# Kernel optimization log

Hardware: AMD Instinct MI355X
Metric: run time of the kernel (lower is better)

## Reference

```python
import jax, jax.numpy as jnp
import numpy as np

B, T, NT = 256, 1024, 96  # batch, max seq len, num_tags (incl. start/end)


def setup_inputs() -> dict:
    key = jax.random.key(0)
    k1, k2, k3 = jax.random.split(key, 3)
    h = jax.random.normal(k1, (B, T, NT), dtype=jnp.float32)
    # lengths in [1, T]; force at least one full-length sequence so max_len == T
    lengths = jax.random.randint(k2, (B,), 1, T + 1).at[0].set(T)
    trans = jax.random.normal(k3, (NT, NT), dtype=jnp.float32)  # trans[to, from]
    return {"h": h, "lengths": lengths, "trans": trans}


def reference(h, lengths, trans):
    # CRF forward algorithm (log partition function), masked for variable lengths.
    Bb, Tt, nt = h.shape
    start_tag, end_tag = nt - 2, nt - 1  # start_tag=-2, end_tag=-1
    mask = jnp.arange(Tt)[None, :] < lengths[:, None]  # [B, T]

    score0 = jnp.full((Bb, nt), -10000.0, dtype=h.dtype).at[:, start_tag].set(0.0)

    def step(score, xs):
        h_t, m_t = xs  # h_t: [B, NT], m_t: [B]
        # score[b, j] (prev tag j) + trans[i, j] + emit h_t[b, i] -> [B, NT(i), NT(j)]
        s = score[:, None, :] + trans[None, :, :] + h_t[:, :, None]
        s = jax.nn.logsumexp(s, axis=2)  # [B, NT]
        score = jnp.where(m_t[:, None], s, score)
        return score, None

    score, _ = jax.lax.scan(step, score0, (jnp.swapaxes(h, 0, 1), mask.T))
    # transition into end tag, then final logsumexp over tags -> [B]
    return jax.nn.logsumexp(score + trans[end_tag][None, :], axis=1)
```

## Files before the change

### kernel.cpp

```cpp
#include <hip/hip_runtime.h>

#define Bb 256
#define Tt 1024
#define NT 96
#define PF 8

__global__ __launch_bounds__(256, 1) void crf_fwd_kernel(
    const float* __restrict__ h,
    const int*   __restrict__ lengths,
    const float* __restrict__ trans,
    float* __restrict__ out)
{
    const int b    = blockIdx.x;
    const int tid  = threadIdx.x;
    const int i    = tid >> 1;
    const int q    = tid & 1;
    const int L    = lengths[b];
    const bool active = (i < NT);
    const int wave = tid >> 6;

    __shared__ float p_lds[2][128];
    __shared__ float fin[4];

    float E[48];
    if (active) {
        const float* tr = trans + i * NT + q * 48;
        #pragma unroll
        for (int k = 0; k < 48; ++k) E[k] = __expf(tr[k]);
    } else {
        #pragma unroll
        for (int k = 0; k < 48; ++k) E[k] = 0.0f;
    }

    if (tid < 128) p_lds[0][tid] = (tid == NT - 2) ? 1.0f : 0.0f;

    const float* hb = h + (size_t)b * Tt * NT;

    float hp[PF];
    #pragma unroll
    for (int k = 0; k < PF; ++k)
        hp[k] = active ? hb[(size_t)k * NT + i] : 0.0f;

    const float c  = 4.0f;
    const float Kc = __expf(-c);
    float M = 0.0f;
    float p_keep = 0.0f;

    __syncthreads();

    int cur = 0;
    for (int tb = 0; tb < Tt; tb += PF) {
        #pragma unroll
        for (int k = 0; k < PF; ++k) {
            const int t = tb + k;

            const float p0 = p_lds[cur][0];

            const float4* pv = reinterpret_cast<const float4*>(p_lds[cur] + q * 48);
            float a0 = 0.f, a1 = 0.f, a2 = 0.f, a3 = 0.f;
            #pragma unroll
            for (int m = 0; m < 12; ++m) {
                const float4 p4 = pv[m];
                a0 = fmaf(E[4*m+0], p4.x, a0);
                a1 = fmaf(E[4*m+1], p4.y, a1);
                a2 = fmaf(E[4*m+2], p4.z, a2);
                a3 = fmaf(E[4*m+3], p4.w, a3);
            }
            float v = (a0 + a1) + (a2 + a3);
            v += __shfl_xor(v, 1, 64);

            const float eh = __expf(hp[k]);
            int tn = t + PF; if (tn > Tt - 1) tn = Tt - 1;
            hp[k] = active ? hb[(size_t)tn * NT + i] : 0.0f;

            const float u  = (t == 0) ? 1.0f : Kc * __builtin_amdgcn_rcpf(p0);
            const float w  = v * eh;
            const bool msk = (t < L);
            const float pn = msk ? (w * u) : p_keep;
            M -= msk ? __logf(u) : 0.0f;
            p_keep = pn;

            const int nxt = cur ^ 1;
            if (active && q == 0) p_lds[nxt][i] = pn;

            __syncthreads();
            cur = nxt;
        }
    }

    float term = (active && q == 0) ? p_keep * __expf(trans[(NT - 1) * NT + i]) : 0.0f;
    #pragma unroll
    for (int s = 1; s < 64; s <<= 1) term += __shfl_xor(term, s, 64);
    if ((tid & 63) == 0) fin[wave] = term;
    __syncthreads();
    if (tid == 0) out[b] = M + __logf(fin[0] + fin[1] + fin[2] + fin[3]);
}

extern "C" void kernel_launch(void* const* d_in, const int* in_sizes, int n_in,
                              void* d_out, int out_size, void* d_ws, size_t ws_size,
                              hipStream_t stream) {
    const float* h       = (const float*)d_in[0];
    const int*   lengths = (const int*)d_in[1];
    const float* trans   = (const float*)d_in[2];
    float*       out     = (float*)d_out;
    (void)in_sizes; (void)n_in; (void)out_size; (void)d_ws; (void)ws_size;

    crf_fwd_kernel<<<Bb, 256, 0, stream>>>(h, lengths, trans, out);
}
```

Measured before the change: 405.5 us.

## Batch 16 sequences per wave with bf16 MFMA recurrence and exp prepass

Replaces the per-batch 256-thread FMA recurrence with a single-wave kernel that advances 16 sequences together. Each step is a bf16 MFMA matrix product of the exponentiated transition matrix against the probability vectors held in LDS. Renormalisation happens only every 16 steps, and the emissions are exponentiated in a separate prepass into workspace when one is available. This removes the block-wide barrier per step and the scalar dot products, but the grid drops to 16 one-wave blocks, the bf16 truncation adds precision loss, and the prepass adds a full extra pass over h.

Measured after the change: 783.6 us. 1.93x slower.

```diff
diff --git a/kernel.cpp b/kernel.cpp
--- a/kernel.cpp
+++ b/kernel.cpp
@@ -3,97 +3,173 @@
 #define Bb 256
 #define Tt 1024
 #define NT 96
-#define PF 8
+#define CH 16
+#define CSTR 120
 
-__global__ __launch_bounds__(256, 1) void crf_fwd_kernel(
-    const float* __restrict__ h,
-    const int*   __restrict__ lengths,
-    const float* __restrict__ trans,
-    float* __restrict__ out)
-{
-    const int b    = blockIdx.x;
-    const int tid  = threadIdx.x;
-    const int i    = tid >> 1;
-    const int q    = tid & 1;
-    const int L    = lengths[b];
-    const bool active = (i < NT);
-    const int wave = tid >> 6;
+typedef __attribute__((ext_vector_type(8))) short bf16x8;
+typedef __attribute__((ext_vector_type(4))) float f32x4;
 
-    __shared__ float p_lds[2][128];
-    __shared__ float fin[4];
+__device__ __forceinline__ unsigned short bf16_rne(float f) {
+    unsigned int b = __float_as_uint(f);
+    b += 0x7FFFu + ((b >> 16) & 1u);
+    return (unsigned short)(b >> 16);
+}
 
-    float E[48];
-    if (active) {
-        const float* tr = trans + i * NT + q * 48;
+__global__ void exp_prepass(const float4* __restrict__ src, float4* __restrict__ dst, int n4) {
+    int idx = blockIdx.x * blockDim.x + threadIdx.x;
+    int stride = gridDim.x * blockDim.x;
+    for (int i = idx; i < n4; i += stride) {
+        float4 v = src[i];
+        dst[i] = make_float4(__expf(v.x), __expf(v.y), __expf(v.z), __expf(v.w));
+    }
+}
+
+template <bool PRE>
+__global__ __attribute__((amdgpu_flat_work_group_size(64, 64),
+                          amdgpu_waves_per_eu(1, 1)))
+void crf_mfma_kernel(const float* __restrict__ hsrc,
+                     const int* __restrict__ lengths,
+                     const float* __restrict__ trans,
+                     float* __restrict__ out) {
+    const int b0   = blockIdx.x * CH;
+    const int lane = threadIdx.x;
+    const int c    = lane & 15;
+    const int g    = lane >> 4;
+    const int L    = lengths[b0 + c];
+
+    __shared__ __align__(16) short pbuf[CH * CSTR];
+
+    bf16x8 afrag[6][3];
+    #pragma unroll
+    for (int mt = 0; mt < 6; ++mt) {
+        const float* row = trans + (16 * mt + c) * NT;
         #pragma unroll
-        for (int k = 0; k < 48; ++k) E[k] = __expf(tr[k]);
-    } else {
-        #pragma unroll
-        for (int k = 0; k < 48; ++k) E[k] = 0.0f;
-    }
-
-    if (tid < 128) p_lds[0][tid] = (tid == NT - 2) ? 1.0f : 0.0f;
-
-    const float* hb = h + (size_t)b * Tt * NT;
-
-    float hp[PF];
-    #pragma unroll
-    for (int k = 0; k < PF; ++k)
-        hp[k] = active ? hb[(size_t)k * NT + i] : 0.0f;
-
-    const float c  = 4.0f;
-    const float Kc = __expf(-c);
-    float M = 0.0f;
-    float p_keep = 0.0f;
-
-    __syncthreads();
-
-    int cur = 0;
-    for (int tb = 0; tb < Tt; tb += PF) {
-        #pragma unroll
-        for (int k = 0; k < PF; ++k) {
-            const int t = tb + k;
-
-            const float p0 = p_lds[cur][0];
-
-            const float4* pv = reinterpret_cast<const float4*>(p_lds[cur] + q * 48);
-            float a0 = 0.f, a1 = 0.f, a2 = 0.f, a3 = 0.f;
-            #pragma unroll
-            for (int m = 0; m < 12; ++m) {
-                const float4 p4 = pv[m];
-                a0 = fmaf(E[4*m+0], p4.x, a0);
-                a1 = fmaf(E[4*m+1], p4.y, a1);
-                a2 = fmaf(E[4*m+2], p4.z, a2);
-                a3 = fmaf(E[4*m+3], p4.w, a3);
-            }
-            float v = (a0 + a1) + (a2 + a3);
-            v += __shfl_xor(v, 1, 64);
-
-            const float eh = __expf(hp[k]);
-            int tn = t + PF; if (tn > Tt - 1) tn = Tt - 1;
-            hp[k] = active ? hb[(size_t)tn * NT + i] : 0.0f;
-
-            const float u  = (t == 0) ? 1.0f : Kc * __builtin_amdgcn_rcpf(p0);
-            const float w  = v * eh;
-            const bool msk = (t < L);
-            const float pn = msk ? (w * u) : p_keep;
-            M -= msk ? __logf(u) : 0.0f;
-            p_keep = pn;
-
-            const int nxt = cur ^ 1;
-            if (active && q == 0) p_lds[nxt][i] = pn;
-
-            __syncthreads();
-            cur = nxt;
+        for (int kt = 0; kt < 3; ++kt) {
+            const float4 t0 = *(const float4*)(row + 32 * kt + 8 * g);
+            const float4 t1 = *(const float4*)(row + 32 * kt + 8 * g + 4);
+            bf16x8 f;
+            f[0] = (short)bf16_rne(__expf(t0.x) * 0.001953125f);
+            f[1] = (short)bf16_rne(__expf(t0.y) * 0.001953125f);
+            f[2] = (short)bf16_rne(__expf(t0.z) * 0.001953125f);
+            f[3] = (short)bf16_rne(__expf(t0.w) * 0.001953125f);
+            f[4] = (short)bf16_rne(__expf(t1.x) * 0.001953125f);
+            f[5] = (short)bf16_rne(__expf(t1.y) * 0.001953125f);
+            f[6] = (short)bf16_rne(__expf(t1.z) * 0.001953125f);
+            f[7] = (short)bf16_rne(__expf(t1.w) * 0.001953125f);
+            afrag[mt][kt] = f;
         }
     }
 
-    float term = (active && q == 0) ? p_keep * __expf(trans[(NT - 1) * NT + i]) : 0.0f;
+    float wC[6][4];
     #pragma unroll
-    for (int s = 1; s < 64; s <<= 1) term += __shfl_xor(term, s, 64);
-    if ((tid & 63) == 0) fin[wave] = term;
-    __syncthreads();
-    if (tid == 0) out[b] = M + __logf(fin[0] + fin[1] + fin[2] + fin[3]);
+    for (int mt = 0; mt < 6; ++mt)
+        #pragma unroll
+        for (int r = 0; r < 4; ++r) wC[mt][r] = 0.0f;
+    if (g == 3) wC[5][2] = 1.0f;
+
+    #pragma unroll
+    for (int mt = 0; mt < 6; ++mt) {
+        unsigned int p01 = (__float_as_uint(wC[mt][1]) & 0xFFFF0000u) |
+                           (__float_as_uint(wC[mt][0]) >> 16);
+        unsigned int p23 = (__float_as_uint(wC[mt][3]) & 0xFFFF0000u) |
+                           (__float_as_uint(wC[mt][2]) >> 16);
+        *(uint2*)&pbuf[c * CSTR + 16 * mt + 4 * g] = make_uint2(p01, p23);
+    }
+
+    const float* hb = hsrc + ((size_t)(b0 + c) * Tt) * NT + 4 * g;
+    float4 hpA[6], hpB[6];
+    #pragma unroll
+    for (int mt = 0; mt < 6; ++mt) hpA[mt] = *(const float4*)(hb + (size_t)0 * NT + 16 * mt);
+    #pragma unroll
+    for (int mt = 0; mt < 6; ++mt) hpB[mt] = *(const float4*)(hb + (size_t)1 * NT + 16 * mt);
+
+    float Mloc = 0.0f;
+
+#define STEPX(HP, T_)                                                          \
+    {                                                                          \
+        bf16x8 bfr[3];                                                         \
+        _Pragma("unroll")                                                      \
+        for (int kt = 0; kt < 3; ++kt)                                         \
+            bfr[kt] = *(const bf16x8*)&pbuf[c * CSTR + 32 * kt + 8 * g];       \
+        f32x4 acc[6];                                                          \
+        _Pragma("unroll")                                                      \
+        for (int mt = 0; mt < 6; ++mt) {                                       \
+            f32x4 a = {0.f, 0.f, 0.f, 0.f};                                    \
+            a = __builtin_amdgcn_mfma_f32_16x16x32_bf16(afrag[mt][0], bfr[0], a, 0, 0, 0); \
+            a = __builtin_amdgcn_mfma_f32_16x16x32_bf16(afrag[mt][1], bfr[1], a, 0, 0, 0); \
+            a = __builtin_amdgcn_mfma_f32_16x16x32_bf16(afrag[mt][2], bfr[2], a, 0, 0, 0); \
+            acc[mt] = a;                                                       \
+        }                                                                      \
+        const bool msk = ((T_) < L);                                           \
+        _Pragma("unroll")                                                      \
+        for (int mt = 0; mt < 6; ++mt) {                                       \
+            const float e0 = PRE ? HP[mt].x : __expf(HP[mt].x);                \
+            const float e1 = PRE ? HP[mt].y : __expf(HP[mt].y);                \
+            const float e2 = PRE ? HP[mt].z : __expf(HP[mt].z);                \
+            const float e3 = PRE ? HP[mt].w : __expf(HP[mt].w);                \
+            wC[mt][0] = msk ? acc[mt][0] * e0 : wC[mt][0];                     \
+            wC[mt][1] = msk ? acc[mt][1] * e1 : wC[mt][1];                     \
+            wC[mt][2] = msk ? acc[mt][2] * e2 : wC[mt][2];                     \
+            wC[mt][3] = msk ? acc[mt][3] * e3 : wC[mt][3];                     \
+        }                                                                      \
+        if (((T_) & 15) == 15) {                                               \
+            float mx = wC[0][0];                                               \
+            _Pragma("unroll")                                                  \
+            for (int mt = 0; mt < 6; ++mt) {                                   \
+                mx = fmaxf(mx, wC[mt][0]); mx = fmaxf(mx, wC[mt][1]);          \
+                mx = fmaxf(mx, wC[mt][2]); mx = fmaxf(mx, wC[mt][3]);          \
+            }                                                                  \
+            mx = fmaxf(mx, __shfl_xor(mx, 16, 64));                            \
+            mx = fmaxf(mx, __shfl_xor(mx, 32, 64));                            \
+            const float ui = __builtin_amdgcn_rcpf(mx);                        \
+            Mloc -= __logf(ui);   \
+            _Pragma("unroll")                                                  \
+            for (int mt = 0; mt < 6; ++mt) {                                   \
+                wC[mt][0] *= ui; wC[mt][1] *= ui;                              \
+                wC[mt][2] *= ui; wC[mt][3] *= ui;                              \
+            }                                                                  \
+        }                                                                      \
+        _Pragma("unroll")                                                      \
+        for (int mt = 0; mt < 6; ++mt) {                                       \
+            unsigned int p01 = (__float_as_uint(wC[mt][1]) & 0xFFFF0000u) |    \
+                               (__float_as_uint(wC[mt][0]) >> 16);             \
+            unsigned int p23 = (__float_as_uint(wC[mt][3]) & 0xFFFF0000u) |    \
+                               (__float_as_uint(wC[mt][2]) >> 16);             \
+            *(uint2*)&pbuf[c * CSTR + 16 * mt + 4 * g] = make_uint2(p01, p23); \
+        }                                                                      \
+    }
+
+    for (int t = 0; t < Tt; t += 2) {
+        STEPX(hpA, t);
+        {
+            const size_t tn = (size_t)((t + 2 > Tt - 1) ? (Tt - 1) : (t + 2));
+            #pragma unroll
+            for (int mt = 0; mt < 6; ++mt)
+                hpA[mt] = *(const float4*)(hb + tn * NT + 16 * mt);
+        }
+        STEPX(hpB, t + 1);
+        {
+            const size_t tn = (size_t)((t + 3 > Tt - 1) ? (Tt - 1) : (t + 3));
+            #pragma unroll
+            for (int mt = 0; mt < 6; ++mt)
+                hpB[mt] = *(const float4*)(hb + tn * NT + 16 * mt);
+        }
+    }
+#undef STEPX
+
+    float ft = 0.0f;
+    #pragma unroll
+    for (int mt = 0; mt < 6; ++mt) {
+        const float4 e4 = *(const float4*)(trans + 95 * NT + 16 * mt + 4 * g);
+        ft += wC[mt][0] * __expf(e4.x);
+        ft += wC[mt][1] * __expf(e4.y);
+        ft += wC[mt][2] * __expf(e4.z);
+        ft += wC[mt][3] * __expf(e4.w);
+    }
+    ft += __shfl_xor(ft, 16, 64);
+    ft += __shfl_xor(ft, 32, 64);
+    if (lane < CH)
+        out[b0 + lane] = Mloc + 6.23832462503951f * (float)L + __logf(ft);
 }
 
 extern "C" void kernel_launch(void* const* d_in, const int* in_sizes, int n_in,
@@ -103,7 +179,14 @@
     const int*   lengths = (const int*)d_in[1];
     const float* trans   = (const float*)d_in[2];
     float*       out     = (float*)d_out;
-    (void)in_sizes; (void)n_in; (void)out_size; (void)d_ws; (void)ws_size;
+    (void)in_sizes; (void)n_in; (void)out_size;
 
-    crf_fwd_kernel<<<Bb, 256, 0, stream>>>(h, lengths, trans, out);
+    const size_t need = (size_t)Bb * Tt * NT * sizeof(float);
+    if (ws_size >= need) {
+        const int n4 = Bb * Tt * NT / 4;
+        exp_prepass<<<2048, 256, 0, stream>>>((const float4*)h, (float4*)d_ws, n4);
+        crf_mfma_kernel<true><<<Bb / CH, 64, 0, stream>>>((const float*)d_ws, lengths, trans, out);
+    } else {
+        crf_mfma_kernel<false><<<Bb / CH, 64, 0, stream>>>(h, lengths, trans, out);
+    }
 }
```
